# Kernel optimization log

Hardware: AMD Instinct MI355X
Metric: run time of the kernel (lower is better)

## Reference

```python
import jax, jax.numpy as jnp
import numpy as np

HEADS = 16
D_MODEL = 1024
D_HEAD = D_MODEL // HEADS


def setup_inputs() -> dict:
    key = jax.random.key(0)
    ks = jax.random.split(key, 12)
    B, S = 4, 2048
    scale = D_MODEL ** -0.5
    inp = {
        "q": jax.random.normal(ks[0], (B, S, D_MODEL), jnp.float32),
        "k": jax.random.normal(ks[1], (B, S, D_MODEL), jnp.float32),
        "v": jax.random.normal(ks[2], (B, S, D_MODEL), jnp.float32),
        # causal mask: True = masked position
        "mask": jnp.triu(jnp.ones((S, S), bool), k=1)[None].repeat(B, axis=0),
        "wq": jax.random.normal(ks[3], (D_MODEL, D_MODEL), jnp.float32) * scale,
        "bq": jnp.zeros((D_MODEL,), jnp.float32),
        "wk": jax.random.normal(ks[4], (D_MODEL, D_MODEL), jnp.float32) * scale,
        "bk": jnp.zeros((D_MODEL,), jnp.float32),
        "wv": jax.random.normal(ks[5], (D_MODEL, D_MODEL), jnp.float32) * scale,
        "bv": jnp.zeros((D_MODEL,), jnp.float32),
        "wo": jax.random.normal(ks[6], (D_MODEL, D_MODEL), jnp.float32) * scale,
        "bo": jnp.zeros((D_MODEL,), jnp.float32),
    }
    return inp


def _split_head(x):
    B, S, _ = x.shape
    return x.reshape(B, S, HEADS, D_HEAD).transpose(0, 2, 1, 3)  # [B,H,S,D]


def reference(q, k, v, mask, wq, bq, wk, bk, wv, bv, wo, bo):
    # linear projections (torch Linear: x @ W^T + b)
    qh = _split_head(q @ wq.T + bq) * (D_HEAD ** -0.5)
    kh = _split_head(k @ wk.T + bk)
    vh = _split_head(v @ wv.T + bv)
    # scores [B,H,Sq,Sk]
    scores = jnp.einsum("bhqd,bhkd->bhqk", qh, kh)
    scores = jnp.where(mask[:, None, :, :], -1e20, scores)
    weights = jax.nn.softmax(scores, axis=-1)  # dropout p=0 in eval
    ctx = jnp.einsum("bhqk,bhkd->bhqd", weights, vh)
    B, H, S, D = ctx.shape
    ctx = ctx.transpose(0, 2, 1, 3).reshape(B, S, H * D)
    return ctx @ wo.T + bo
```

## Files before the change

### kernel.cpp

```cpp
#include <hip/hip_runtime.h>
#include <hip/hip_bf16.h>
#include <cstdint>
#include <cstddef>

typedef unsigned short u16;
typedef unsigned int u32;
using short8  = __attribute__((ext_vector_type(8))) short;
using f32x4   = __attribute__((ext_vector_type(4))) float;
using f32x16  = __attribute__((ext_vector_type(16))) float;
using u32x4   = __attribute__((ext_vector_type(4))) u32;

#define SCALE_Q 0.18033688011112043f

#define WAITVM(N) asm volatile("s_waitcnt vmcnt(" #N ")" ::: "memory")
#define LGKM0    asm volatile("s_waitcnt lgkmcnt(0)" ::: "memory")
#define BARX     __builtin_amdgcn_s_barrier()
#define SCHED0   __builtin_amdgcn_sched_barrier(0)

__device__ inline u16 f2bf(float f) {
  return __builtin_bit_cast(u16, __float2bfloat16(f));
}

__device__ inline u32 cvt_pk_bf16(float a, float b) {
  u32 r;
  asm("v_cvt_pk_bf16_f32 %0, %1, %2" : "=v"(r) : "v"(a), "v"(b));
  return r;
}

__device__ inline f32x4 mfma16(short8 a, short8 b, f32x4 c) {
  return __builtin_amdgcn_mfma_f32_16x16x32_bf16(a, b, c, 0, 0, 0);
}
__device__ inline f32x16 mfma32(short8 a, short8 b, f32x16 c) {
  return __builtin_amdgcn_mfma_f32_32x32x16_bf16(a, b, c, 0, 0, 0);
}

__device__ inline void gload16(const void* g, void* l) {
  __builtin_amdgcn_global_load_lds(
      (const __attribute__((address_space(1))) void*)g,
      (__attribute__((address_space(3))) void*)l,
      16, 0, 0);
}

__global__ __launch_bounds__(256)
void prep(const float* __restrict__ wq, const float* __restrict__ wk,
          const float* __restrict__ wv, const float* __restrict__ wo,
          u16* __restrict__ Wb) {
  const int c = blockIdx.x * 256 + threadIdx.x;
  const int m = c >> 17;
  const size_t off = (size_t)(c & 131071) * 8;
  const float* src = (m == 0) ? wq : (m == 1) ? wk : (m == 2) ? wv : wo;
  const float sc = (m == 0) ? SCALE_Q : 1.f;
  f32x4 a = *(const f32x4*)(src + off);
  f32x4 b = *(const f32x4*)(src + off + 4);
  short8 vv;
#pragma unroll
  for (int j = 0; j < 4; ++j) { vv[j] = (short)f2bf(a[j] * sc); vv[4 + j] = (short)f2bf(b[j] * sc); }
  *(short8*)&Wb[(size_t)m * 1048576 + off] = vv;
}

struct GemmArgs {
  const float* qf; const float* kf; const float* vf;
  const u16* ctx; const u16* Wb;
  const float* bq; const float* bk; const float* bv; const float* bo;
  u16* Qs; u16* Ks; u16* Vs; float* out;
};

template<bool FUSED>
__global__ __launch_bounds__(256, FUSED ? 2 : 3)
void gemm_proj(GemmArgs ga, int modeBase) {
  const int mode = modeBase + blockIdx.z;
  const int bx = blockIdx.x;
  const int bm = ((bx & 7) << 3) | (bx >> 3);
  const int bn = blockIdx.y;
  const int tid = threadIdx.x;
  const int w = tid >> 6, lane = tid & 63;
  const int wr = w >> 1, wc = w & 1;
  const int l15 = lane & 15, g = lane >> 4;

  const float* Af = (mode == 0) ? ga.qf : (mode == 1) ? ga.kf : ga.vf;
  const u16*   Am = ga.ctx;
  const u16*   Wm = ga.Wb + (size_t)mode * 1048576;
  const float* bias = (mode == 0) ? ga.bq : (mode == 1) ? ga.bk : (mode == 2) ? ga.bv : ga.bo;

  __shared__ u16 As[2][128 * 64];
  __shared__ u16 Bs[2][128 * 64];

  f32x4 acc[4][4] = {};
  const int m0 = bm * 128, n0 = bn * 128;

  const int r_lo = lane >> 3;
  const int sc8 = ((lane & 7) ^ (lane >> 3)) * 8;

  auto stageB = [&](int k0, int slot) {
#pragma unroll
    for (int i = 0; i < 4; ++i)
      gload16(Wm + (size_t)(n0 + i * 32 + w * 8 + r_lo) * 1024 + k0 + sc8,
              &Bs[slot][i * 2048 + w * 512]);
  };
  auto stageA_lds = [&](int k0, int slot) {
#pragma unroll
    for (int i = 0; i < 4; ++i)
      gload16(Am + (size_t)(m0 + i * 32 + w * 8 + r_lo) * 1024 + k0 + sc8,
              &As[slot][i * 2048 + w * 512]);
  };
  auto loadA = [&](int k0, f32x4 (&r)[8]) {
#pragma unroll
    for (int i = 0; i < 4; ++i) {
      const float* src = Af + (size_t)(m0 + i * 32 + w * 8 + r_lo) * 1024 + k0 + sc8;
      r[2 * i]     = *(const f32x4*)(src);
      r[2 * i + 1] = *(const f32x4*)(src + 4);
    }
  };
  auto writeA = [&](f32x4 (&r)[8], int slot) {
#pragma unroll
    for (int i = 0; i < 4; ++i) {
      u32x4 wv;
      wv[0] = cvt_pk_bf16(r[2 * i][0], r[2 * i][1]);
      wv[1] = cvt_pk_bf16(r[2 * i][2], r[2 * i][3]);
      wv[2] = cvt_pk_bf16(r[2 * i + 1][0], r[2 * i + 1][1]);
      wv[3] = cvt_pk_bf16(r[2 * i + 1][2], r[2 * i + 1][3]);
      *(u32x4*)&As[slot][i * 2048 + w * 512 + lane * 8] = wv;
    }
  };

  auto compute = [&](int slot) {
#pragma unroll
    for (int kk = 0; kk < 2; ++kk) {
      short8 av[4], bv4[4];
#pragma unroll
      for (int mi = 0; mi < 4; ++mi) {
        const int row = wr * 64 + mi * 16 + l15;
        av[mi] = *(const short8*)&As[slot][row * 64 + ((((kk << 2) | g)) ^ (row & 7)) * 8];
      }
#pragma unroll
      for (int ni = 0; ni < 4; ++ni) {
        const int row = wc * 64 + ni * 16 + l15;
        bv4[ni] = *(const short8*)&Bs[slot][row * 64 + ((((kk << 2) | g)) ^ (row & 7)) * 8];
      }
#pragma unroll
      for (int mi = 0; mi < 4; ++mi)
#pragma unroll
        for (int ni = 0; ni < 4; ++ni)
          acc[mi][ni] = mfma16(av[mi], bv4[ni], acc[mi][ni]);
    }
  };

  if (FUSED) {
    f32x4 rA[8], rB[8];
    loadA(0, rA);  stageB(0, 0);
    loadA(64, rB); stageB(64, 1);
    WAITVM(12);
    writeA(rA, 0);
    LGKM0;
    BARX; SCHED0;
    for (int tt = 0; tt < 14; tt += 2) {
      compute(0);
      BARX; SCHED0;
      WAITVM(0);
      writeA(rB, 1);
      LGKM0;
      loadA((tt + 2) * 64, rA); stageB((tt + 2) * 64, 0);
      BARX; SCHED0;
      compute(1);
      BARX; SCHED0;
      WAITVM(0);
      writeA(rA, 0);
      LGKM0;
      if (tt + 3 < 16) { loadA((tt + 3) * 64, rB); stageB((tt + 3) * 64, 1); }
      BARX; SCHED0;
    }
    compute(0);
    BARX; SCHED0;
    WAITVM(0);
    writeA(rB, 1);
    LGKM0;
    BARX; SCHED0;
    compute(1);
  } else {
    stageA_lds(0, 0);  stageB(0, 0);
    stageA_lds(64, 1); stageB(64, 1);
#pragma unroll 2
    for (int t = 0; t < 14; ++t) {
      WAITVM(8);
      BARX; SCHED0;
      compute(t & 1);
      BARX; SCHED0;
      stageA_lds((t + 2) * 64, t & 1); stageB((t + 2) * 64, t & 1);
    }
    WAITVM(8);
    BARX; SCHED0;
    compute(0);
    WAITVM(0);
    BARX; SCHED0;
    compute(1);
  }

  float bvals[4];
#pragma unroll
  for (int ni = 0; ni < 4; ++ni)
    bvals[ni] = bias[n0 + wc * 64 + ni * 16 + l15] * ((mode == 0) ? SCALE_Q : 1.f);

  if (mode == 3) {
#pragma unroll
    for (int mi = 0; mi < 4; ++mi)
#pragma unroll
      for (int ni = 0; ni < 4; ++ni)
#pragma unroll
        for (int r = 0; r < 4; ++r) {
          const int m = m0 + wr * 64 + mi * 16 + g * 4 + r;
          const int n = n0 + wc * 64 + ni * 16 + l15;
          ga.out[(size_t)m * 1024 + n] = acc[mi][ni][r] + bvals[ni];
        }
  } else {
    u16* O = (mode == 0) ? ga.Qs : (mode == 1) ? ga.Ks : ga.Vs;
#pragma unroll
    for (int mi = 0; mi < 4; ++mi)
#pragma unroll
      for (int ni = 0; ni < 4; ++ni)
#pragma unroll
        for (int r = 0; r < 4; ++r) {
          const int m = m0 + wr * 64 + mi * 16 + g * 4 + r;
          const int n = n0 + wc * 64 + ni * 16 + l15;
          const int b = m >> 11, s = m & 2047, hh = n >> 6, d = n & 63;
          const float val = acc[mi][ni][r] + bvals[ni];
          const size_t base = (size_t)(b * 16 + hh) * 131072;
          size_t idx;
          if (mode == 2) {
            const int sp = (s & ~12) | ((s & 4) << 1) | ((s & 8) >> 1);
            const int kt = sp >> 5, w5 = sp & 31;
            const int j = ((d >> 5) << 1) | (w5 >> 4);
            const int hi2 = (w5 >> 3) & 1, e = w5 & 7;
            idx = base + (size_t)kt * 2048 + j * 512 + hi2 * 256 + (d & 31) * 8 + e;
          } else {
            const int s32 = s >> 5, l31 = s & 31;
            const int t2 = d >> 4, hi2 = (d >> 3) & 1, e = d & 7;
            idx = base + (size_t)s32 * 2048 + t2 * 512 + hi2 * 256 + l31 * 8 + e;
          }
          O[idx] = f2bf(val);
        }
  }
}

__global__ __launch_bounds__(256)
void attn_fwd(const u16* __restrict__ Qs, const u16* __restrict__ Ks,
              const u16* __restrict__ Vs, u16* __restrict__ ctx) {
  const int bh = blockIdx.x;
  const int qt = 15 - blockIdx.y;
  const int tid = threadIdx.x;
  const int w = tid >> 6, lane = tid & 63;
  const int l31 = lane & 31, hi = lane >> 5;

  const u16* Qb = Qs + (size_t)bh * 131072;
  const u16* Kb = Ks + (size_t)bh * 131072;
  const u16* Vb = Vs + (size_t)bh * 131072;
  const int b = bh >> 4, hh = bh & 15;

  const int qw0 = qt * 128 + w * 32;
  const int nktw = (qw0 >> 5) + 1;
  const int nktmax = qt * 4 + 4;
  const int qrow = qw0 + l31;

  __shared__ u16 Klds[2][2048];
  __shared__ u16 Vlds[2][2048];

  auto stageKV = [&](int kt, int slot) {
    const size_t toff = (size_t)kt * 2048 + (w * 64 + lane) * 8;
    gload16(Kb + toff, &Klds[slot][w * 512]);
    gload16(Vb + toff, &Vlds[slot][w * 512]);
  };

  stageKV(0, 0);
  stageKV(1, 1);
  __builtin_amdgcn_sched_barrier(0);

  short8 qf[4];
  {
    const u16* qp = Qb + (size_t)(qw0 >> 5) * 2048 + lane * 8;
#pragma unroll
    for (int t = 0; t < 4; ++t) qf[t] = *(const short8*)(qp + t * 512);
  }
  __builtin_amdgcn_sched_barrier(0);

  f32x16 oacc0 = {}, oacc1 = {};
  float lsum = 0.f;

  for (int kt = 0; kt < nktmax; ++kt) {
    const int slot = kt & 1;
    if (kt + 1 < nktmax) { WAITVM(2); } else { WAITVM(0); }
    __builtin_amdgcn_s_barrier();
    __builtin_amdgcn_sched_barrier(0);

    short8 kf[4], vf[4];
#pragma unroll
    for (int t = 0; t < 4; ++t) {
      kf[t] = *(const short8*)&Klds[slot][t * 512 + lane * 8];
      vf[t] = *(const short8*)&Vlds[slot][t * 512 + lane * 8];
    }

    f32x16 st = {};
    __builtin_amdgcn_s_setprio(1);
    st = mfma32(kf[0], qf[0], st);
    st = mfma32(kf[1], qf[1], st);
    st = mfma32(kf[2], qf[2], st);
    st = mfma32(kf[3], qf[3], st);
    __builtin_amdgcn_s_setprio(0);

    if (kt >= nktw - 1) {
#pragma unroll
      for (int r = 0; r < 16; ++r) {
        const int ka = kt * 32 + (r & 3) + 8 * (r >> 2) + 4 * hi;
        if (ka > qrow) st[r] = -1e30f;
      }
    }

    float p[16];
#pragma unroll
    for (int r = 0; r < 16; ++r) p[r] = __builtin_amdgcn_exp2f(st[r]);
    {
      float s0 = (p[0] + p[1]) + (p[2] + p[3]);
      float s1 = (p[4] + p[5]) + (p[6] + p[7]);
      float s2 = (p[8] + p[9]) + (p[10] + p[11]);
      float s3 = (p[12] + p[13]) + (p[14] + p[15]);
      lsum += (s0 + s1) + (s2 + s3);
    }
    u32x4 a0, a1;
#pragma unroll
    for (int v2 = 0; v2 < 4; ++v2) {
      a0[v2] = cvt_pk_bf16(p[2 * v2], p[2 * v2 + 1]);
      a1[v2] = cvt_pk_bf16(p[8 + 2 * v2], p[9 + 2 * v2]);
    }
    const short8 pb0 = __builtin_bit_cast(short8, a0);
    const short8 pb1 = __builtin_bit_cast(short8, a1);
    __builtin_amdgcn_s_setprio(1);
    oacc0 = mfma32(vf[0], pb0, oacc0);
    oacc0 = mfma32(vf[1], pb1, oacc0);
    oacc1 = mfma32(vf[2], pb0, oacc1);
    oacc1 = mfma32(vf[3], pb1, oacc1);
    __builtin_amdgcn_s_setprio(0);

    __builtin_amdgcn_s_barrier();
    __builtin_amdgcn_sched_barrier(0);
    if (kt + 2 < nktmax) stageKV(kt + 2, slot);
  }

  lsum += __shfl_xor(lsum, 32);
  const float inv = __builtin_amdgcn_rcpf(lsum);

  u16* crow = ctx + ((size_t)(b * 2048 + qrow)) * 1024 + hh * 64;
#pragma unroll
  for (int r = 0; r < 16; r += 2) {
    const int d0 = (r & 3) + 8 * (r >> 2) + 4 * hi;
    *(u32*)&crow[d0]      = cvt_pk_bf16(oacc0[r] * inv, oacc0[r + 1] * inv);
    *(u32*)&crow[32 + d0] = cvt_pk_bf16(oacc1[r] * inv, oacc1[r + 1] * inv);
  }
}

extern "C" void kernel_launch(void* const* d_in, const int* in_sizes, int n_in,
                              void* d_out, int out_size, void* d_ws, size_t ws_size,
                              hipStream_t stream) {
  const float* q  = (const float*)d_in[0];
  const float* k  = (const float*)d_in[1];
  const float* v  = (const float*)d_in[2];
  const float* wq = (const float*)d_in[4];
  const float* bq = (const float*)d_in[5];
  const float* wk = (const float*)d_in[6];
  const float* bk = (const float*)d_in[7];
  const float* wv = (const float*)d_in[8];
  const float* bv = (const float*)d_in[9];
  const float* wo = (const float*)d_in[10];
  const float* bo = (const float*)d_in[11];

  char* ws = (char*)d_ws;
  const size_t WBSZ = (size_t)4 * 1048576 * sizeof(u16);
  const size_t SZ   = (size_t)64 * 131072 * sizeof(u16);
  u16* Wb  = (u16*)(ws);
  u16* Qs  = (u16*)(ws + WBSZ);
  u16* Ks  = (u16*)(ws + WBSZ + SZ);
  u16* Vs  = (u16*)(ws + WBSZ + 2 * SZ);
  u16* ctx = (u16*)(ws + WBSZ + 3 * SZ);

  GemmArgs ga;
  ga.qf = q; ga.kf = k; ga.vf = v; ga.ctx = ctx; ga.Wb = Wb;
  ga.bq = bq; ga.bk = bk; ga.bv = bv; ga.bo = bo;
  ga.Qs = Qs; ga.Ks = Ks; ga.Vs = Vs; ga.out = (float*)d_out;

  prep<<<dim3(2048), dim3(256), 0, stream>>>(wq, wk, wv, wo, Wb);
  gemm_proj<true><<<dim3(64, 8, 3), dim3(256), 0, stream>>>(ga, 0);
  attn_fwd<<<dim3(64, 16), dim3(256), 0, stream>>>(Qs, Ks, Vs, ctx);
  gemm_proj<false><<<dim3(64, 8, 1), dim3(256), 0, stream>>>(ga, 3);
}
```

Baseline: 171.9 us.

## Triple-buffer B tiles in fused projection GEMM and overlap loads with compute

The fused fp32-input projection GEMM now keeps three LDS slots for the weight tile, so the next B tile's async load can be issued before the current compute. This removes one barrier per half-step and the full vmcnt(0) drains, replacing them with partial waits. The non-fused path's launch bounds drop from 3 to 2 blocks per CU, and the extra 16KB of LDS shared by both instantiations may reduce occupancy there. The slot rotation and vmcnt counts must match the issue order exactly, or stale data will be read.

```diff
diff --git a/kernel.cpp b/kernel.cpp
--- a/kernel.cpp
+++ b/kernel.cpp
@@ -66,7 +66,7 @@
 };
 
 template<bool FUSED>
-__global__ __launch_bounds__(256, FUSED ? 2 : 3)
+__global__ __launch_bounds__(256, 2)
 void gemm_proj(GemmArgs ga, int modeBase) {
   const int mode = modeBase + blockIdx.z;
   const int bx = blockIdx.x;
@@ -83,7 +83,7 @@
   const float* bias = (mode == 0) ? ga.bq : (mode == 1) ? ga.bk : (mode == 2) ? ga.bv : ga.bo;
 
   __shared__ u16 As[2][128 * 64];
-  __shared__ u16 Bs[2][128 * 64];
+  __shared__ u16 Bs[3][128 * 64];
 
   f32x4 acc[4][4] = {};
   const int m0 = bm * 128, n0 = bn * 128;
@@ -123,19 +123,19 @@
     }
   };
 
-  auto compute = [&](int slot) {
+  auto compute = [&](int aslot, int bslot) {
 #pragma unroll
     for (int kk = 0; kk < 2; ++kk) {
       short8 av[4], bv4[4];
 #pragma unroll
       for (int mi = 0; mi < 4; ++mi) {
         const int row = wr * 64 + mi * 16 + l15;
-        av[mi] = *(const short8*)&As[slot][row * 64 + ((((kk << 2) | g)) ^ (row & 7)) * 8];
+        av[mi] = *(const short8*)&As[aslot][row * 64 + ((((kk << 2) | g)) ^ (row & 7)) * 8];
       }
 #pragma unroll
       for (int ni = 0; ni < 4; ++ni) {
         const int row = wc * 64 + ni * 16 + l15;
-        bv4[ni] = *(const short8*)&Bs[slot][row * 64 + ((((kk << 2) | g)) ^ (row & 7)) * 8];
+        bv4[ni] = *(const short8*)&Bs[bslot][row * 64 + ((((kk << 2) | g)) ^ (row & 7)) * 8];
       }
 #pragma unroll
       for (int mi = 0; mi < 4; ++mi)
@@ -147,35 +147,39 @@
 
   if (FUSED) {
     f32x4 rA[8], rB[8];
-    loadA(0, rA);  stageB(0, 0);
-    loadA(64, rB); stageB(64, 1);
-    WAITVM(12);
+    stageB(0, 0); stageB(64, 1);
+    loadA(0, rA); loadA(64, rB);
+    WAITVM(8);
     writeA(rA, 0);
     LGKM0;
+
+    int bs0 = 0;
+    for (int p = 0; p < 14; p += 2) {
+      int bs1 = bs0 + 1; if (bs1 == 3) bs1 = 0;
+      int bs2 = bs1 + 1; if (bs2 == 3) bs2 = 0;
+      BARX; SCHED0;
+      stageB((p + 2) * 64, bs2);
+      compute(0, bs0);
+      WAITVM(4);
+      writeA(rB, 1);
+      loadA((p + 2) * 64, rA);
+      LGKM0;
+      BARX; SCHED0;
+      stageB((p + 3) * 64, bs0);
+      compute(1, bs1);
+      WAITVM(4);
+      writeA(rA, 0);
+      loadA((p + 3) * 64, rB);
+      LGKM0;
+      bs0 = bs2;
+    }
     BARX; SCHED0;
-    for (int tt = 0; tt < 14; tt += 2) {
-      compute(0);
-      BARX; SCHED0;
-      WAITVM(0);
-      writeA(rB, 1);
-      LGKM0;
-      loadA((tt + 2) * 64, rA); stageB((tt + 2) * 64, 0);
-      BARX; SCHED0;
-      compute(1);
-      BARX; SCHED0;
-      WAITVM(0);
-      writeA(rA, 0);
-      LGKM0;
-      if (tt + 3 < 16) { loadA((tt + 3) * 64, rB); stageB((tt + 3) * 64, 1); }
-      BARX; SCHED0;
-    }
-    compute(0);
-    BARX; SCHED0;
+    compute(0, bs0);
     WAITVM(0);
     writeA(rB, 1);
     LGKM0;
     BARX; SCHED0;
-    compute(1);
+    compute(1, (bs0 + 1 == 3) ? 0 : bs0 + 1);
   } else {
     stageA_lds(0, 0);  stageB(0, 0);
     stageA_lds(64, 1); stageB(64, 1);
@@ -183,16 +187,16 @@
     for (int t = 0; t < 14; ++t) {
       WAITVM(8);
       BARX; SCHED0;
-      compute(t & 1);
+      compute(t & 1, t & 1);
       BARX; SCHED0;
       stageA_lds((t + 2) * 64, t & 1); stageB((t + 2) * 64, t & 1);
     }
     WAITVM(8);
     BARX; SCHED0;
-    compute(0);
+    compute(0, 0);
     WAITVM(0);
     BARX; SCHED0;
-    compute(1);
+    compute(1, 1);
   }
 
   float bvals[4];
```

Measured after the change: 169.9 us. Within noise of the previous version (-1.2%).
